# Optimization experiments

Measured on AMD Instinct MI355X. Metric: run time of the kernel, lower is better.

Reference implementation:

```python
import jax, jax.numpy as jnp
import numpy as np

D = 768          # hidden_size
M = 8            # num_patchmerges
B = 16
S = 2048         # non-CLF tokens


def setup_inputs() -> dict:
    key = jax.random.key(0)
    ks = jax.random.split(key, 12)
    std = 0.02
    tokens = jax.random.normal(ks[0], (B, 1 + S, D), dtype=jnp.float32)
    lengths = jnp.maximum(jax.random.randint(ks[1], (B,), 0, S), 1).astype(jnp.int64)
    # PatchMerger: learned queries + layernorm params
    q = jax.random.normal(ks[2], (M, D), dtype=jnp.float32) * std
    ln_scale = jnp.ones((D,), dtype=jnp.float32)
    ln_bias = jnp.zeros((D,), dtype=jnp.float32)
    # mlp1: Linear(3D, D) -> GELU -> Linear(D, D)
    w1a = jax.random.normal(ks[3], (3 * D, D), dtype=jnp.float32) * std
    b1a = jnp.zeros((D,), dtype=jnp.float32)
    w2a = jax.random.normal(ks[4], (D, D), dtype=jnp.float32) * std
    b2a = jnp.zeros((D,), dtype=jnp.float32)
    # mlp2: Linear((1+M)D, D) -> GELU -> Linear(D, D)
    w1b = jax.random.normal(ks[5], ((1 + M) * D, D), dtype=jnp.float32) * std
    b1b = jnp.zeros((D,), dtype=jnp.float32)
    w2b = jax.random.normal(ks[6], (D, D), dtype=jnp.float32) * std
    b2b = jnp.zeros((D,), dtype=jnp.float32)
    return dict(tokens=tokens, lengths=lengths, q=q, ln_scale=ln_scale,
                ln_bias=ln_bias, w1a=w1a, b1a=b1a, w2a=w2a, b2a=b2a,
                w1b=w1b, b1b=b1b, w2b=w2b, b2b=b2b)


def _hpmlp(x, w1, b1, w2, b2):
    h = jax.nn.gelu(x @ w1 + b1, approximate=False)  # dropout=0 -> identity
    return h @ w2 + b2


def _layernorm(x, scale, bias, eps=1e-5):
    mu = jnp.mean(x, axis=-1, keepdims=True)
    var = jnp.var(x, axis=-1, keepdims=True)
    return (x - mu) * jax.lax.rsqrt(var + eps) * scale + bias


def reference(tokens, lengths, q, ln_scale, ln_bias,
              w1a, b1a, w2a, b2a, w1b, b1b, w2b, b2b):
    clf = tokens[:, 0]            # [B, D]
    x = tokens[:, 1:]             # [B, S, D]
    mask = jnp.arange(S)[None, :] < lengths[:, None]   # [B, S]
    mf = mask[..., None].astype(x.dtype)

    # fixed path: masked mean / max / min over valid tokens
    denom = lengths.astype(x.dtype)[:, None]
    mean_p = jnp.sum(x * mf, axis=1) / denom
    max_p = jnp.max(jnp.where(mask[..., None], x, -jnp.inf), axis=1)
    min_p = jnp.min(jnp.where(mask[..., None], x, jnp.inf), axis=1)
    pooled_trad = jnp.concatenate([mean_p, max_p, min_p], axis=-1)  # [B, 3D]
    out_fixed = _hpmlp(pooled_trad, w1a, b1a, w2a, b2a)

    # learned path: PatchMerger (masked attention from M learned queries)
    xn = _layernorm(x, ln_scale, ln_bias)
    scores = jnp.einsum('md,bsd->bms', q, xn) / jnp.sqrt(jnp.asarray(D, x.dtype))
    scores = jnp.where(mask[:, None, :], scores, -jnp.inf)
    attn = jax.nn.softmax(scores, axis=-1)                # [B, M, S]
    merged = jnp.einsum('bms,bsd->bmd', attn, x)          # [B, M, D]
    pooled_learn = jnp.concatenate([merged.reshape(B, M * D), clf], axis=-1)
    out_learn = _hpmlp(pooled_learn, w1b, b1b, w2b, b2b)

    return jnp.concatenate([out_fixed, out_learn], axis=-1)  # [B, 2D]
```

## Files before the change

### kernel.cpp

```cpp
#include <hip/hip_runtime.h>
#include <math.h>

#define SD 768
#define SB 16
#define SM 8
#define SS 2048
#define TOK_ROW 2049
#define NEG_INF (-__builtin_inff())

#define OFF_PPOOL   0
#define OFF_PO      1179648
#define OFF_PML     4325376
#define OFF_PTRAD   4333568
#define OFF_PLEARN  4370432
#define OFF_P1A     4481024
#define OFF_P1B     4702208
#define OFF_HA      5365760
#define OFF_HB      5378048
#define OFF_P2A     5390336
#define OFF_P2B     5464064

__device__ __forceinline__ int clen(int v) { return v < 1 ? 1 : (v > SS ? SS : v); }

__global__ __launch_bounds__(256, 2) void k1_flash(
    const float* __restrict__ tokens, const int* __restrict__ lengths,
    const float* __restrict__ q, const float* __restrict__ lns,
    const float* __restrict__ lnb, float* __restrict__ ppool,
    float* __restrict__ pO, float* __restrict__ pml) {
  int c = blockIdx.x, b = blockIdx.y;
  int len = clen(lengths[b]);
  int c0 = c * 64;
  if (c0 >= len) return;
  int tid = threadIdx.x, w = tid >> 6, lane = tid & 63;
  int mm = lane & 7;

  __shared__ float p_lds[4][16][8];
  __shared__ float pool_lds[4][3][SD];
  __shared__ float O_lds[SM][SD];
  __shared__ float mx_lds[8];

  {
    float* pf = &p_lds[0][0][0];
    for (int i = tid; i < 512; i += 256) pf[i] = NEG_INF;
  }

  float4 qr[8][3];
  float qs1sel, qbsel;
  {
    float4 l4[3], lb4[3];
    #pragma unroll
    for (int g = 0; g < 3; ++g) {
      l4[g] = *(const float4*)(lns + g * 256 + lane * 4);
      lb4[g] = *(const float4*)(lnb + g * 256 + lane * 4);
    }
    float qs1r[8], qbr[8];
    #pragma unroll
    for (int m = 0; m < 8; ++m) {
      float s1 = 0.f, sb = 0.f;
      #pragma unroll
      for (int g = 0; g < 3; ++g) {
        float4 qv = *(const float4*)(q + m * SD + g * 256 + lane * 4);
        float4 qs;
        qs.x = qv.x * l4[g].x; qs.y = qv.y * l4[g].y;
        qs.z = qv.z * l4[g].z; qs.w = qv.w * l4[g].w;
        qr[m][g] = qs;
        s1 += qs.x + qs.y + qs.z + qs.w;
        sb += qv.x * lb4[g].x + qv.y * lb4[g].y + qv.z * lb4[g].z + qv.w * lb4[g].w;
      }
      #pragma unroll
      for (int o = 32; o; o >>= 1) { s1 += __shfl_xor(s1, o, 64); sb += __shfl_xor(sb, o, 64); }
      qs1r[m] = s1; qbr[m] = sb;
    }
    qs1sel = qs1r[0]; qbsel = qbr[0];
    #pragma unroll
    for (int m = 1; m < 8; ++m) {
      qs1sel = (mm == m) ? qs1r[m] : qs1sel;
      qbsel = (mm == m) ? qbr[m] : qbsel;
    }
  }
  __syncthreads();

  float psum[12], pmax[12], pmin[12];
  #pragma unroll
  for (int j = 0; j < 12; ++j) { psum[j] = 0.f; pmax[j] = NEG_INF; pmin[j] = -NEG_INF; }

  int srow = c0 + w * 16;
  int smax = len - srow; if (smax > 16) smax = 16; if (smax < 0) smax = 0;
  const float* xrow = tokens + ((size_t)b * TOK_ROW + 1 + srow) * SD;

  float4 nx0 = {}, nx1 = {}, nx2 = {};
  if (smax > 0) {
    nx0 = *(const float4*)(xrow + lane * 4);
    nx1 = *(const float4*)(xrow + 256 + lane * 4);
    nx2 = *(const float4*)(xrow + 512 + lane * 4);
  }
  for (int i = 0; i < smax; ++i) {
    float4 x0 = nx0, x1 = nx1, x2 = nx2;
    if (i + 1 < smax) {
      const float* xq = xrow + (size_t)(i + 1) * SD;
      nx0 = *(const float4*)(xq + lane * 4);
      nx1 = *(const float4*)(xq + 256 + lane * 4);
      nx2 = *(const float4*)(xq + 512 + lane * 4);
    }
    float xv[12] = {x0.x, x0.y, x0.z, x0.w, x1.x, x1.y, x1.z, x1.w,
                    x2.x, x2.y, x2.z, x2.w};
    float s1 = 0.f, s2 = 0.f;
    #pragma unroll
    for (int j = 0; j < 12; ++j) {
      float v = xv[j];
      psum[j] += v;
      pmax[j] = fmaxf(pmax[j], v);
      pmin[j] = fminf(pmin[j], v);
      s1 += v;
      s2 += v * v;
    }
    float d[8];
    #pragma unroll
    for (int m = 0; m < 8; ++m) {
      float4 a0 = qr[m][0], a1 = qr[m][1], a2 = qr[m][2];
      d[m] = a0.x * xv[0] + a0.y * xv[1] + a0.z * xv[2] + a0.w * xv[3]
           + a1.x * xv[4] + a1.y * xv[5] + a1.z * xv[6] + a1.w * xv[7]
           + a2.x * xv[8] + a2.y * xv[9] + a2.z * xv[10] + a2.w * xv[11];
    }
    #pragma unroll
    for (int o = 1; o <= 4; o <<= 1)
      #pragma unroll
      for (int m = 0; m < 8; ++m) d[m] += __shfl_xor(d[m], o, 64);
    float u = d[0];
    #pragma unroll
    for (int m = 1; m < 8; ++m) u = (mm == m) ? d[m] : u;
    #pragma unroll
    for (int o = 8; o <= 32; o <<= 1) {
      u += __shfl_xor(u, o, 64);
      s1 += __shfl_xor(s1, o, 64);
      s2 += __shfl_xor(s2, o, 64);
    }
    #pragma unroll
    for (int o = 1; o <= 4; o <<= 1) { s1 += __shfl_xor(s1, o, 64); s2 += __shfl_xor(s2, o, 64); }
    float mu = s1 * (1.f / 768.f);
    float var = s2 * (1.f / 768.f) - mu * mu;
    float rstd = rsqrtf(var + 1e-5f);
    float sc = (rstd * u - rstd * mu * qs1sel + qbsel) * 0.03608439182435161f;
    if (lane < 8) p_lds[w][i][lane] = sc;
  }

  #pragma unroll
  for (int g = 0; g < 3; ++g) {
    int dd = g * 256 + lane * 4;
    *(float4*)&pool_lds[w][0][dd] = make_float4(psum[g*4], psum[g*4+1], psum[g*4+2], psum[g*4+3]);
    *(float4*)&pool_lds[w][1][dd] = make_float4(pmax[g*4], pmax[g*4+1], pmax[g*4+2], pmax[g*4+3]);
    *(float4*)&pool_lds[w][2][dd] = make_float4(pmin[g*4], pmin[g*4+1], pmin[g*4+2], pmin[g*4+3]);
  }
  __syncthreads();

  float* pf = &p_lds[0][0][0];
  if (tid < 8) {
    float mxv = NEG_INF;
    for (int r = 0; r < 64; ++r) mxv = fmaxf(mxv, pf[r * 8 + tid]);
    mx_lds[tid] = mxv;
  }
  __syncthreads();
  for (int e = tid; e < 512; e += 256) {
    int m = e & 7;
    pf[e] = __expf(pf[e] - mx_lds[m]);
  }
  __syncthreads();
  if (tid < 8) {
    float lv = 0.f;
    for (int r = 0; r < 64; ++r) lv += pf[r * 8 + tid];
    size_t base = (size_t)(c * SB + b) * 16;
    pml[base + tid] = mx_lds[tid];
    pml[base + 8 + tid] = lv;
  }

  float O[8][12];
  #pragma unroll
  for (int m = 0; m < 8; ++m)
    #pragma unroll
    for (int j = 0; j < 12; ++j) O[m][j] = 0.f;
  float4 a0v = {}, a1v = {}, a2v = {}, b0v = {}, b1v = {}, b2v = {};
  if (smax > 0) {
    a0v = *(const float4*)(xrow + lane * 4);
    a1v = *(const float4*)(xrow + 256 + lane * 4);
    a2v = *(const float4*)(xrow + 512 + lane * 4);
  }
  if (smax > 1) {
    const float* xq = xrow + SD;
    b0v = *(const float4*)(xq + lane * 4);
    b1v = *(const float4*)(xq + 256 + lane * 4);
    b2v = *(const float4*)(xq + 512 + lane * 4);
  }
  for (int i = 0; i < smax; ++i) {
    float4 x0 = a0v, x1 = a1v, x2 = a2v;
    a0v = b0v; a1v = b1v; a2v = b2v;
    if (i + 2 < smax) {
      const float* xq = xrow + (size_t)(i + 2) * SD;
      b0v = *(const float4*)(xq + lane * 4);
      b1v = *(const float4*)(xq + 256 + lane * 4);
      b2v = *(const float4*)(xq + 512 + lane * 4);
    }
    float xv[12] = {x0.x, x0.y, x0.z, x0.w, x1.x, x1.y, x1.z, x1.w,
                    x2.x, x2.y, x2.z, x2.w};
    const float4* pr = (const float4*)&p_lds[w][i][0];
    float4 pa = pr[0], pb = pr[1];
    float pm[8] = {pa.x, pa.y, pa.z, pa.w, pb.x, pb.y, pb.z, pb.w};
    #pragma unroll
    for (int m = 0; m < 8; ++m)
      #pragma unroll
      for (int j = 0; j < 12; ++j) O[m][j] += pm[m] * xv[j];
  }
  #pragma unroll
  for (int r = 0; r < 4; ++r) {
    if (w == r) {
      #pragma unroll
      for (int m = 0; m < 8; ++m)
        #pragma unroll
        for (int g = 0; g < 3; ++g) {
          int dd = g * 256 + lane * 4;
          float4 mine = make_float4(O[m][g*4], O[m][g*4+1], O[m][g*4+2], O[m][g*4+3]);
          if (r == 0) {
            *(float4*)&O_lds[m][dd] = mine;
          } else {
            float4 cur = *(float4*)&O_lds[m][dd];
            cur.x += mine.x; cur.y += mine.y; cur.z += mine.z; cur.w += mine.w;
            *(float4*)&O_lds[m][dd] = cur;
          }
        }
    }
    __syncthreads();
  }

  size_t obase = (size_t)(c * SB + b) * 6144;
  const float* of = &O_lds[0][0];
  for (int j = tid * 4; j < 6144; j += 1024)
    *(float4*)&pO[obase + j] = *(const float4*)&of[j];

  size_t pbase = (size_t)(c * SB + b) * 2304;
  for (int j4 = tid * 4; j4 < 2304; j4 += 1024) {
    int stat = j4 / SD, dd = j4 - stat * SD;
    float4 v0 = *(float4*)&pool_lds[0][stat][dd];
    float4 v1 = *(float4*)&pool_lds[1][stat][dd];
    float4 v2 = *(float4*)&pool_lds[2][stat][dd];
    float4 v3 = *(float4*)&pool_lds[3][stat][dd];
    float4 r;
    if (stat == 0) {
      r.x = v0.x + v1.x + v2.x + v3.x; r.y = v0.y + v1.y + v2.y + v3.y;
      r.z = v0.z + v1.z + v2.z + v3.z; r.w = v0.w + v1.w + v2.w + v3.w;
    } else if (stat == 1) {
      r.x = fmaxf(fmaxf(v0.x, v1.x), fmaxf(v2.x, v3.x));
      r.y = fmaxf(fmaxf(v0.y, v1.y), fmaxf(v2.y, v3.y));
      r.z = fmaxf(fmaxf(v0.z, v1.z), fmaxf(v2.z, v3.z));
      r.w = fmaxf(fmaxf(v0.w, v1.w), fmaxf(v2.w, v3.w));
    } else {
      r.x = fminf(fminf(v0.x, v1.x), fminf(v2.x, v3.x));
      r.y = fminf(fminf(v0.y, v1.y), fminf(v2.y, v3.y));
      r.z = fminf(fminf(v0.z, v1.z), fminf(v2.z, v3.z));
      r.w = fminf(fminf(v0.w, v1.w), fminf(v2.w, v3.w));
    }
    *(float4*)&ppool[pbase + j4] = r;
  }
}

__global__ void k_combine(const float* __restrict__ ppool, const float* __restrict__ pO,
                          const float* __restrict__ pml, const float* __restrict__ tokens,
                          const int* __restrict__ lengths,
                          float* __restrict__ ptrad, float* __restrict__ plearn) {
  int tile = blockIdx.x, b = blockIdx.y;
  int len = clen(lengths[b]);
  int nv = (len + 63) >> 6;
  int tid = threadIdx.x;
  __shared__ float pml_lds[32][16];
  __shared__ float e_lds[32][8];
  __shared__ float Linv_lds[8];
  for (int t = tid; t < nv * 16; t += 256) {
    int cc = t >> 4, j = t & 15;
    pml_lds[cc][j] = pml[(size_t)(cc * SB + b) * 16 + j];
  }
  __syncthreads();
  if (tid < 8) {
    float M = NEG_INF;
    for (int cc = 0; cc < nv; ++cc) M = fmaxf(M, pml_lds[cc][tid]);
    float L = 0.f;
    for (int cc = 0; cc < nv; ++cc) {
      float e = __expf(pml_lds[cc][tid] - M);
      e_lds[cc][tid] = e;
      L += e * pml_lds[cc][8 + tid];
    }
    Linv_lds[tid] = 1.f / L;
  }
  __syncthreads();
  #pragma unroll
  for (int k = 0; k < 4; ++k) {
    int jj = tile * 1024 + k * 256 + tid;
    if (jj < 2304) {
      int stat = jj / SD;
      const float* pp = ppool + jj + (size_t)b * 2304;
      if (stat == 0) {
        float a0 = 0.f, a1 = 0.f, a2 = 0.f, a3 = 0.f;
        int cc = 0;
        for (; cc + 4 <= nv; cc += 4) {
          a0 += pp[(size_t)(cc    ) * SB * 2304];
          a1 += pp[(size_t)(cc + 1) * SB * 2304];
          a2 += pp[(size_t)(cc + 2) * SB * 2304];
          a3 += pp[(size_t)(cc + 3) * SB * 2304];
        }
        for (; cc < nv; ++cc) a0 += pp[(size_t)cc * SB * 2304];
        ptrad[b * 2304 + jj] = ((a0 + a1) + (a2 + a3)) / (float)len;
      } else if (stat == 1) {
        float a0 = NEG_INF, a1 = NEG_INF, a2 = NEG_INF, a3 = NEG_INF;
        int cc = 0;
        for (; cc + 4 <= nv; cc += 4) {
          a0 = fmaxf(a0, pp[(size_t)(cc    ) * SB * 2304]);
          a1 = fmaxf(a1, pp[(size_t)(cc + 1) * SB * 2304]);
          a2 = fmaxf(a2, pp[(size_t)(cc + 2) * SB * 2304]);
          a3 = fmaxf(a3, pp[(size_t)(cc + 3) * SB * 2304]);
        }
        for (; cc < nv; ++cc) a0 = fmaxf(a0, pp[(size_t)cc * SB * 2304]);
        ptrad[b * 2304 + jj] = fmaxf(fmaxf(a0, a1), fmaxf(a2, a3));
      } else {
        float a0 = -NEG_INF, a1 = -NEG_INF, a2 = -NEG_INF, a3 = -NEG_INF;
        int cc = 0;
        for (; cc + 4 <= nv; cc += 4) {
          a0 = fminf(a0, pp[(size_t)(cc    ) * SB * 2304]);
          a1 = fminf(a1, pp[(size_t)(cc + 1) * SB * 2304]);
          a2 = fminf(a2, pp[(size_t)(cc + 2) * SB * 2304]);
          a3 = fminf(a3, pp[(size_t)(cc + 3) * SB * 2304]);
        }
        for (; cc < nv; ++cc) a0 = fminf(a0, pp[(size_t)cc * SB * 2304]);
        ptrad[b * 2304 + jj] = fminf(fminf(a0, a1), fminf(a2, a3));
      }
    } else if (jj < 8448) {
      int t = jj - 2304;
      int m = t / SD;
      const float* po = pO + t + (size_t)b * 6144;
      float a0 = 0.f, a1 = 0.f, a2 = 0.f, a3 = 0.f;
      float a4 = 0.f, a5 = 0.f, a6 = 0.f, a7 = 0.f;
      int cc = 0;
      for (; cc + 8 <= nv; cc += 8) {
        a0 += po[(size_t)(cc    ) * SB * 6144] * e_lds[cc    ][m];
        a1 += po[(size_t)(cc + 1) * SB * 6144] * e_lds[cc + 1][m];
        a2 += po[(size_t)(cc + 2) * SB * 6144] * e_lds[cc + 2][m];
        a3 += po[(size_t)(cc + 3) * SB * 6144] * e_lds[cc + 3][m];
        a4 += po[(size_t)(cc + 4) * SB * 6144] * e_lds[cc + 4][m];
        a5 += po[(size_t)(cc + 5) * SB * 6144] * e_lds[cc + 5][m];
        a6 += po[(size_t)(cc + 6) * SB * 6144] * e_lds[cc + 6][m];
        a7 += po[(size_t)(cc + 7) * SB * 6144] * e_lds[cc + 7][m];
      }
      for (; cc < nv; ++cc) a0 += po[(size_t)cc * SB * 6144] * e_lds[cc][m];
      plearn[b * 6912 + t] = (((a0 + a1) + (a2 + a3)) + ((a4 + a5) + (a6 + a7))) * Linv_lds[m];
    } else {
      int dd = jj - 8448;
      plearn[b * 6912 + 6144 + dd] = tokens[(size_t)b * TOK_ROW * SD + dd];
    }
  }
}

__global__ __launch_bounds__(256) void gemm_partial(
    const float* __restrict__ XA, const float* __restrict__ WA, int ktA, float* __restrict__ PA,
    const float* __restrict__ XB, const float* __restrict__ WB, float* __restrict__ PB) {
  int nt = blockIdx.x, ky = blockIdx.y;
  const float *X, *W; float* P; int kt, ktN;
  if (ky < ktA) { X = XA; W = WA; P = PA; kt = ky; ktN = ktA; }
  else { X = XB; W = WB; P = PB; kt = ky - ktA; ktN = gridDim.y - ktA; }
  int K = ktN * 128;
  int k0 = kt * 128;
  __shared__ __align__(16) float xt[128 * 20];
  __shared__ float red[4][64][17];
  int tid = threadIdx.x;
  int kk = tid & 127, half = tid >> 7;
  #pragma unroll
  for (int u = 0; u < 8; ++u) {
    int b2 = half * 8 + u;
    xt[kk * 20 + b2] = X[b2 * K + k0 + kk];
  }
  __syncthreads();
  int w = tid >> 6, lane = tid & 63;
  int n = nt * 64 + lane;
  float acc[16];
  #pragma unroll
  for (int b2 = 0; b2 < 16; ++b2) acc[b2] = 0.f;
  const float* Wp = W + (size_t)k0 * SD + n;
  #pragma unroll 8
  for (int kj = 0; kj < 32; ++kj) {
    int k = w + kj * 4;
    float wv = Wp[(size_t)k * SD];
    const float4* xr = reinterpret_cast<const float4*>(xt + k * 20);
    float4 a0 = xr[0], a1 = xr[1], a2 = xr[2], a3 = xr[3];
    acc[0] += wv * a0.x; acc[1] += wv * a0.y; acc[2] += wv * a0.z; acc[3] += wv * a0.w;
    acc[4] += wv * a1.x; acc[5] += wv * a1.y; acc[6] += wv * a1.z; acc[7] += wv * a1.w;
    acc[8] += wv * a2.x; acc[9] += wv * a2.y; acc[10] += wv * a2.z; acc[11] += wv * a2.w;
    acc[12] += wv * a3.x; acc[13] += wv * a3.y; acc[14] += wv * a3.z; acc[15] += wv * a3.w;
  }
  #pragma unroll
  for (int b2 = 0; b2 < 16; ++b2) red[w][lane][b2] = acc[b2];
  __syncthreads();
  for (int i = tid; i < 1024; i += 256) {
    int nn = i & 63, b2 = i >> 6;
    float r = red[0][nn][b2] + red[1][nn][b2] + red[2][nn][b2] + red[3][nn][b2];
    P[(size_t)(kt * 16 + b2) * SD + nt * 64 + nn] = r;
  }
}

__global__ void gelu_reduce(const float* __restrict__ PA, const float* __restrict__ b1a,
                            float* __restrict__ HA, const float* __restrict__ PB,
                            const float* __restrict__ b1b, float* __restrict__ HB) {
  int y = blockIdx.y;
  int j = blockIdx.x * 256 + threadIdx.x;
  float r;
  if (y == 0) {
    r = b1a[j % SD];
    #pragma unroll
    for (int kt = 0; kt < 18; ++kt) r += PA[kt * 12288 + j];
    HA[j] = r * 0.5f * (1.f + erff(r * 0.70710678118654752f));
  } else {
    r = b1b[j % SD];
    #pragma unroll
    for (int kt = 0; kt < 54; ++kt) r += PB[kt * 12288 + j];
    HB[j] = r * 0.5f * (1.f + erff(r * 0.70710678118654752f));
  }
}

__global__ void final_reduce(const float* __restrict__ P2A, const float* __restrict__ b2a,
                             const float* __restrict__ P2B, const float* __restrict__ b2b,
                             float* __restrict__ out) {
  int y = blockIdx.y;
  const float* P = y ? P2B : P2A;
  const float* bias = y ? b2b : b2a;
  int j = blockIdx.x * 256 + threadIdx.x;
  float r = bias[j % SD];
  #pragma unroll
  for (int kt = 0; kt < 6; ++kt) r += P[kt * 12288 + j];
  int b = j / SD, nn = j - b * SD;
  out[b * 1536 + y * SD + nn] = r;
}

extern "C" void kernel_launch(void* const* d_in, const int* in_sizes, int n_in,
                              void* d_out, int out_size, void* d_ws, size_t ws_size,
                              hipStream_t stream) {
  const float* tokens = (const float*)d_in[0];
  const int* lengths  = (const int*)d_in[1];
  const float* q      = (const float*)d_in[2];
  const float* lns    = (const float*)d_in[3];
  const float* lnb    = (const float*)d_in[4];
  const float* w1a    = (const float*)d_in[5];
  const float* b1a    = (const float*)d_in[6];
  const float* w2a    = (const float*)d_in[7];
  const float* b2a    = (const float*)d_in[8];
  const float* w1b    = (const float*)d_in[9];
  const float* b1b    = (const float*)d_in[10];
  const float* w2b    = (const float*)d_in[11];
  const float* b2b    = (const float*)d_in[12];
  float* ws  = (float*)d_ws;
  float* out = (float*)d_out;

  float* ppool  = ws + OFF_PPOOL;
  float* pO     = ws + OFF_PO;
  float* pml    = ws + OFF_PML;
  float* ptrad  = ws + OFF_PTRAD;
  float* plearn = ws + OFF_PLEARN;
  float* p1a    = ws + OFF_P1A;
  float* p1b    = ws + OFF_P1B;
  float* ha     = ws + OFF_HA;
  float* hb     = ws + OFF_HB;
  float* p2a    = ws + OFF_P2A;
  float* p2b    = ws + OFF_P2B;

  k1_flash<<<dim3(32, 16), 256, 0, stream>>>(tokens, lengths, q, lns, lnb, ppool, pO, pml);
  k_combine<<<dim3(9, 16), 256, 0, stream>>>(ppool, pO, pml, tokens, lengths, ptrad, plearn);
  gemm_partial<<<dim3(12, 72), 256, 0, stream>>>(ptrad, w1a, 18, p1a, plearn, w1b, p1b);
  gelu_reduce<<<dim3(48, 2), 256, 0, stream>>>(p1a, b1a, ha, p1b, b1b, hb);
  gemm_partial<<<dim3(12, 12), 256, 0, stream>>>(ha, w2a, 6, p2a, hb, w2b, p2b);
  final_reduce<<<dim3(48, 2), 256, 0, stream>>>(p2a, b2a, p2b, b2b, out);
}
```

Before: 232.5 us.

## Fuse combine and MLP stages into one persistent kernel with grid barriers

Merges the combine, first GEMM, GELU reduce, second GEMM and final reduce kernels into a single 864-block kernel. The stages are separated by atomic-counter grid barriers, and the counters are reset by the flash kernel. This removes four kernel launches and their inter-kernel gaps. In exchange it relies on all 864 blocks being co-resident (launch bounds 4 blocks per CU), and most blocks sit idle at the later, smaller stages.

New measurement: 765.7 us. 229% more time.

```diff
diff --git a/kernel.cpp b/kernel.cpp
--- a/kernel.cpp
+++ b/kernel.cpp
@@ -19,15 +19,31 @@
 #define OFF_HB      5378048
 #define OFF_P2A     5390336
 #define OFF_P2B     5464064
+#define OFF_CNT     5537792
+
+#define MEGA_NB 864
 
 __device__ __forceinline__ int clen(int v) { return v < 1 ? 1 : (v > SS ? SS : v); }
+
+__device__ __forceinline__ void gridbar(int* cnt, int target) {
+  __syncthreads();
+  if (threadIdx.x == 0) {
+    __threadfence();
+    __hip_atomic_fetch_add(cnt, 1, __ATOMIC_RELEASE, __HIP_MEMORY_SCOPE_AGENT);
+    while (__hip_atomic_load(cnt, __ATOMIC_ACQUIRE, __HIP_MEMORY_SCOPE_AGENT) < target)
+      __builtin_amdgcn_s_sleep(2);
+    __threadfence();
+  }
+  __syncthreads();
+}
 
 __global__ __launch_bounds__(256, 2) void k1_flash(
     const float* __restrict__ tokens, const int* __restrict__ lengths,
     const float* __restrict__ q, const float* __restrict__ lns,
     const float* __restrict__ lnb, float* __restrict__ ppool,
-    float* __restrict__ pO, float* __restrict__ pml) {
+    float* __restrict__ pO, float* __restrict__ pml, int* __restrict__ cnt) {
   int c = blockIdx.x, b = blockIdx.y;
+  if (c == 0 && b == 0 && threadIdx.x < 4) cnt[threadIdx.x] = 0;
   int len = clen(lengths[b]);
   int c0 = c * 64;
   if (c0 >= len) return;
@@ -261,38 +277,72 @@
   }
 }
 
-__global__ void k_combine(const float* __restrict__ ppool, const float* __restrict__ pO,
-                          const float* __restrict__ pml, const float* __restrict__ tokens,
-                          const int* __restrict__ lengths,
-                          float* __restrict__ ptrad, float* __restrict__ plearn) {
-  int tile = blockIdx.x, b = blockIdx.y;
-  int len = clen(lengths[b]);
-  int nv = (len + 63) >> 6;
-  int tid = threadIdx.x;
-  __shared__ float pml_lds[32][16];
-  __shared__ float e_lds[32][8];
-  __shared__ float Linv_lds[8];
-  for (int t = tid; t < nv * 16; t += 256) {
-    int cc = t >> 4, j = t & 15;
-    pml_lds[cc][j] = pml[(size_t)(cc * SB + b) * 16 + j];
-  }
-  __syncthreads();
-  if (tid < 8) {
-    float M = NEG_INF;
-    for (int cc = 0; cc < nv; ++cc) M = fmaxf(M, pml_lds[cc][tid]);
-    float L = 0.f;
-    for (int cc = 0; cc < nv; ++cc) {
-      float e = __expf(pml_lds[cc][tid] - M);
-      e_lds[cc][tid] = e;
-      L += e * pml_lds[cc][8 + tid];
-    }
-    Linv_lds[tid] = 1.f / L;
-  }
-  __syncthreads();
-  #pragma unroll
-  for (int k = 0; k < 4; ++k) {
-    int jj = tile * 1024 + k * 256 + tid;
-    if (jj < 2304) {
+__device__ __forceinline__ void gemm_tile(const float* __restrict__ X,
+                                          const float* __restrict__ W,
+                                          float* __restrict__ P,
+                                          int kt, int ktN, int nt, int tid,
+                                          float* __restrict__ smem) {
+  float* xt = smem;
+  float* red = smem + 2560;
+  int K = ktN * 128;
+  int k0 = kt * 128;
+  int kk = tid & 127, half = tid >> 7;
+  #pragma unroll
+  for (int u = 0; u < 8; ++u) {
+    int b2 = half * 8 + u;
+    xt[kk * 20 + b2] = X[b2 * K + k0 + kk];
+  }
+  __syncthreads();
+  int w = tid >> 6, lane = tid & 63;
+  int n = nt * 64 + lane;
+  float acc[16];
+  #pragma unroll
+  for (int b2 = 0; b2 < 16; ++b2) acc[b2] = 0.f;
+  const float* Wp = W + (size_t)k0 * SD + n;
+  #pragma unroll 8
+  for (int kj = 0; kj < 32; ++kj) {
+    int k = w + kj * 4;
+    float wv = Wp[(size_t)k * SD];
+    const float4* xr = reinterpret_cast<const float4*>(xt + k * 20);
+    float4 a0 = xr[0], a1 = xr[1], a2 = xr[2], a3 = xr[3];
+    acc[0] += wv * a0.x; acc[1] += wv * a0.y; acc[2] += wv * a0.z; acc[3] += wv * a0.w;
+    acc[4] += wv * a1.x; acc[5] += wv * a1.y; acc[6] += wv * a1.z; acc[7] += wv * a1.w;
+    acc[8] += wv * a2.x; acc[9] += wv * a2.y; acc[10] += wv * a2.z; acc[11] += wv * a2.w;
+    acc[12] += wv * a3.x; acc[13] += wv * a3.y; acc[14] += wv * a3.z; acc[15] += wv * a3.w;
+  }
+  #pragma unroll
+  for (int b2 = 0; b2 < 16; ++b2) red[(w * 64 + lane) * 17 + b2] = acc[b2];
+  __syncthreads();
+  for (int i = tid; i < 1024; i += 256) {
+    int nn = i & 63, b2 = i >> 6;
+    float r = red[nn * 17 + b2] + red[(64 + nn) * 17 + b2]
+            + red[(128 + nn) * 17 + b2] + red[(192 + nn) * 17 + b2];
+    P[(size_t)(kt * 16 + b2) * SD + nt * 64 + nn] = r;
+  }
+}
+
+__global__ __launch_bounds__(256, 4) void k2_mega(
+    const float* __restrict__ ppool, const float* __restrict__ pO,
+    const float* __restrict__ pml, const float* __restrict__ tokens,
+    const int* __restrict__ lengths,
+    const float* __restrict__ w1a, const float* __restrict__ b1a,
+    const float* __restrict__ w2a, const float* __restrict__ b2a,
+    const float* __restrict__ w1b, const float* __restrict__ b1b,
+    const float* __restrict__ w2b, const float* __restrict__ b2b,
+    float* __restrict__ ptrad, float* __restrict__ plearn,
+    float* __restrict__ p1a, float* __restrict__ p1b,
+    float* __restrict__ ha, float* __restrict__ hb,
+    float* __restrict__ p2a, float* __restrict__ p2b,
+    float* __restrict__ out, int* __restrict__ cnt) {
+  __shared__ __align__(16) float smem[6912];
+  int bid = blockIdx.x, tid = threadIdx.x;
+
+  if (bid < 576) {
+    int b = bid / 36, t36 = bid % 36;
+    int len = clen(lengths[b]);
+    int nv = (len + 63) >> 6;
+    int jj = t36 * 256 + tid;
+    if (t36 < 9) {
       int stat = jj / SD;
       const float* pp = ppool + jj + (size_t)b * 2304;
       if (stat == 0) {
@@ -329,109 +379,93 @@
         for (; cc < nv; ++cc) a0 = fminf(a0, pp[(size_t)cc * SB * 2304]);
         ptrad[b * 2304 + jj] = fminf(fminf(a0, a1), fminf(a2, a3));
       }
-    } else if (jj < 8448) {
-      int t = jj - 2304;
-      int m = t / SD;
-      const float* po = pO + t + (size_t)b * 6144;
+    } else if (t36 < 33) {
+      float* pml_l = smem;
+      float* e_l   = smem + 512;
+      float* linv  = smem + 768;
+      for (int t = tid; t < nv * 16; t += 256)
+        pml_l[t] = pml[(size_t)((t >> 4) * SB + b) * 16 + (t & 15)];
+      __syncthreads();
+      if (tid < 8) {
+        float M = NEG_INF;
+        for (int cc = 0; cc < nv; ++cc) M = fmaxf(M, pml_l[cc * 16 + tid]);
+        float L = 0.f;
+        for (int cc = 0; cc < nv; ++cc) {
+          float e = __expf(pml_l[cc * 16 + tid] - M);
+          e_l[cc * 8 + tid] = e;
+          L += e * pml_l[cc * 16 + 8 + tid];
+        }
+        linv[tid] = 1.f / L;
+      }
+      __syncthreads();
+      int t_ = jj - 2304;
+      int m = t_ / SD;
+      const float* po = pO + t_ + (size_t)b * 6144;
       float a0 = 0.f, a1 = 0.f, a2 = 0.f, a3 = 0.f;
       float a4 = 0.f, a5 = 0.f, a6 = 0.f, a7 = 0.f;
       int cc = 0;
       for (; cc + 8 <= nv; cc += 8) {
-        a0 += po[(size_t)(cc    ) * SB * 6144] * e_lds[cc    ][m];
-        a1 += po[(size_t)(cc + 1) * SB * 6144] * e_lds[cc + 1][m];
-        a2 += po[(size_t)(cc + 2) * SB * 6144] * e_lds[cc + 2][m];
-        a3 += po[(size_t)(cc + 3) * SB * 6144] * e_lds[cc + 3][m];
-        a4 += po[(size_t)(cc + 4) * SB * 6144] * e_lds[cc + 4][m];
-        a5 += po[(size_t)(cc + 5) * SB * 6144] * e_lds[cc + 5][m];
-        a6 += po[(size_t)(cc + 6) * SB * 6144] * e_lds[cc + 6][m];
-        a7 += po[(size_t)(cc + 7) * SB * 6144] * e_lds[cc + 7][m];
+        a0 += po[(size_t)(cc    ) * SB * 6144] * e_l[(cc    ) * 8 + m];
+        a1 += po[(size_t)(cc + 1) * SB * 6144] * e_l[(cc + 1) * 8 + m];
+        a2 += po[(size_t)(cc + 2) * SB * 6144] * e_l[(cc + 2) * 8 + m];
+        a3 += po[(size_t)(cc + 3) * SB * 6144] * e_l[(cc + 3) * 8 + m];
+        a4 += po[(size_t)(cc + 4) * SB * 6144] * e_l[(cc + 4) * 8 + m];
+        a5 += po[(size_t)(cc + 5) * SB * 6144] * e_l[(cc + 5) * 8 + m];
+        a6 += po[(size_t)(cc + 6) * SB * 6144] * e_l[(cc + 6) * 8 + m];
+        a7 += po[(size_t)(cc + 7) * SB * 6144] * e_l[(cc + 7) * 8 + m];
       }
-      for (; cc < nv; ++cc) a0 += po[(size_t)cc * SB * 6144] * e_lds[cc][m];
-      plearn[b * 6912 + t] = (((a0 + a1) + (a2 + a3)) + ((a4 + a5) + (a6 + a7))) * Linv_lds[m];
+      for (; cc < nv; ++cc) a0 += po[(size_t)cc * SB * 6144] * e_l[cc * 8 + m];
+      plearn[b * 6912 + t_] = (((a0 + a1) + (a2 + a3)) + ((a4 + a5) + (a6 + a7))) * linv[m];
     } else {
       int dd = jj - 8448;
       plearn[b * 6912 + 6144 + dd] = tokens[(size_t)b * TOK_ROW * SD + dd];
     }
   }
-}
-
-__global__ __launch_bounds__(256) void gemm_partial(
-    const float* __restrict__ XA, const float* __restrict__ WA, int ktA, float* __restrict__ PA,
-    const float* __restrict__ XB, const float* __restrict__ WB, float* __restrict__ PB) {
-  int nt = blockIdx.x, ky = blockIdx.y;
-  const float *X, *W; float* P; int kt, ktN;
-  if (ky < ktA) { X = XA; W = WA; P = PA; kt = ky; ktN = ktA; }
-  else { X = XB; W = WB; P = PB; kt = ky - ktA; ktN = gridDim.y - ktA; }
-  int K = ktN * 128;
-  int k0 = kt * 128;
-  __shared__ __align__(16) float xt[128 * 20];
-  __shared__ float red[4][64][17];
-  int tid = threadIdx.x;
-  int kk = tid & 127, half = tid >> 7;
-  #pragma unroll
-  for (int u = 0; u < 8; ++u) {
-    int b2 = half * 8 + u;
-    xt[kk * 20 + b2] = X[b2 * K + k0 + kk];
-  }
-  __syncthreads();
-  int w = tid >> 6, lane = tid & 63;
-  int n = nt * 64 + lane;
-  float acc[16];
-  #pragma unroll
-  for (int b2 = 0; b2 < 16; ++b2) acc[b2] = 0.f;
-  const float* Wp = W + (size_t)k0 * SD + n;
-  #pragma unroll 8
-  for (int kj = 0; kj < 32; ++kj) {
-    int k = w + kj * 4;
-    float wv = Wp[(size_t)k * SD];
-    const float4* xr = reinterpret_cast<const float4*>(xt + k * 20);
-    float4 a0 = xr[0], a1 = xr[1], a2 = xr[2], a3 = xr[3];
-    acc[0] += wv * a0.x; acc[1] += wv * a0.y; acc[2] += wv * a0.z; acc[3] += wv * a0.w;
-    acc[4] += wv * a1.x; acc[5] += wv * a1.y; acc[6] += wv * a1.z; acc[7] += wv * a1.w;
-    acc[8] += wv * a2.x; acc[9] += wv * a2.y; acc[10] += wv * a2.z; acc[11] += wv * a2.w;
-    acc[12] += wv * a3.x; acc[13] += wv * a3.y; acc[14] += wv * a3.z; acc[15] += wv * a3.w;
-  }
-  #pragma unroll
-  for (int b2 = 0; b2 < 16; ++b2) red[w][lane][b2] = acc[b2];
-  __syncthreads();
-  for (int i = tid; i < 1024; i += 256) {
-    int nn = i & 63, b2 = i >> 6;
-    float r = red[0][nn][b2] + red[1][nn][b2] + red[2][nn][b2] + red[3][nn][b2];
-    P[(size_t)(kt * 16 + b2) * SD + nt * 64 + nn] = r;
-  }
-}
-
-__global__ void gelu_reduce(const float* __restrict__ PA, const float* __restrict__ b1a,
-                            float* __restrict__ HA, const float* __restrict__ PB,
-                            const float* __restrict__ b1b, float* __restrict__ HB) {
-  int y = blockIdx.y;
-  int j = blockIdx.x * 256 + threadIdx.x;
-  float r;
-  if (y == 0) {
-    r = b1a[j % SD];
-    #pragma unroll
-    for (int kt = 0; kt < 18; ++kt) r += PA[kt * 12288 + j];
-    HA[j] = r * 0.5f * (1.f + erff(r * 0.70710678118654752f));
-  } else {
-    r = b1b[j % SD];
-    #pragma unroll
-    for (int kt = 0; kt < 54; ++kt) r += PB[kt * 12288 + j];
-    HB[j] = r * 0.5f * (1.f + erff(r * 0.70710678118654752f));
-  }
-}
-
-__global__ void final_reduce(const float* __restrict__ P2A, const float* __restrict__ b2a,
-                             const float* __restrict__ P2B, const float* __restrict__ b2b,
-                             float* __restrict__ out) {
-  int y = blockIdx.y;
-  const float* P = y ? P2B : P2A;
-  const float* bias = y ? b2b : b2a;
-  int j = blockIdx.x * 256 + threadIdx.x;
-  float r = bias[j % SD];
-  #pragma unroll
-  for (int kt = 0; kt < 6; ++kt) r += P[kt * 12288 + j];
-  int b = j / SD, nn = j - b * SD;
-  out[b * 1536 + y * SD + nn] = r;
+  gridbar(cnt + 0, MEGA_NB);
+
+  {
+    int nt = bid % 12, ky = bid / 12;
+    if (ky < 18) gemm_tile(ptrad, w1a, p1a, ky, 18, nt, tid, smem);
+    else         gemm_tile(plearn, w1b, p1b, ky - 18, 54, nt, tid, smem);
+  }
+  gridbar(cnt + 1, MEGA_NB);
+
+  if (bid < 96) {
+    int y = bid / 48;
+    int j = (bid % 48) * 256 + tid;
+    float r;
+    if (y == 0) {
+      r = b1a[j % SD];
+      #pragma unroll
+      for (int kt = 0; kt < 18; ++kt) r += p1a[kt * 12288 + j];
+      ha[j] = r * 0.5f * (1.f + erff(r * 0.70710678118654752f));
+    } else {
+      r = b1b[j % SD];
+      #pragma unroll
+      for (int kt = 0; kt < 54; ++kt) r += p1b[kt * 12288 + j];
+      hb[j] = r * 0.5f * (1.f + erff(r * 0.70710678118654752f));
+    }
+  }
+  gridbar(cnt + 2, MEGA_NB);
+
+  if (bid < 144) {
+    int nt = bid % 12, ky = bid / 12;
+    if (ky < 6) gemm_tile(ha, w2a, p2a, ky, 6, nt, tid, smem);
+    else        gemm_tile(hb, w2b, p2b, ky - 6, 6, nt, tid, smem);
+  }
+  gridbar(cnt + 3, MEGA_NB);
+
+  if (bid < 96) {
+    int y = bid / 48;
+    const float* P = y ? p2b : p2a;
+    const float* bias = y ? b2b : b2a;
+    int j = (bid % 48) * 256 + tid;
+    float r = bias[j % SD];
+    #pragma unroll
+    for (int kt = 0; kt < 6; ++kt) r += P[kt * 12288 + j];
+    int b = j / SD, nn = j - b * SD;
+    out[b * 1536 + y * SD + nn] = r;
+  }
 }
 
 extern "C" void kernel_launch(void* const* d_in, const int* in_sizes, int n_in,
@@ -464,11 +498,11 @@
   float* hb     = ws + OFF_HB;
   float* p2a    = ws + OFF_P2A;
   float* p2b    = ws + OFF_P2B;
-
-  k1_flash<<<dim3(32, 16), 256, 0, stream>>>(tokens, lengths, q, lns, lnb, ppool, pO, pml);
-  k_combine<<<dim3(9, 16), 256, 0, stream>>>(ppool, pO, pml, tokens, lengths, ptrad, plearn);
-  gemm_partial<<<dim3(12, 72), 256, 0, stream>>>(ptrad, w1a, 18, p1a, plearn, w1b, p1b);
-  gelu_reduce<<<dim3(48, 2), 256, 0, stream>>>(p1a, b1a, ha, p1b, b1b, hb);
-  gemm_partial<<<dim3(12, 12), 256, 0, stream>>>(ha, w2a, 6, p2a, hb, w2b, p2b);
-  final_reduce<<<dim3(48, 2), 256, 0, stream>>>(p2a, b2a, p2b, b2b, out);
+  int*   cnt    = (int*)(ws + OFF_CNT);
+
+  k1_flash<<<dim3(32, 16), 256, 0, stream>>>(tokens, lengths, q, lns, lnb, ppool, pO, pml, cnt);
+  k2_mega<<<dim3(MEGA_NB), 256, 0, stream>>>(ppool, pO, pml, tokens, lengths,
+                                             w1a, b1a, w2a, b2a, w1b, b1b, w2b, b2b,
+                                             ptrad, plearn, p1a, p1b, ha, hb, p2a, p2b,
+                                             out, cnt);
 }
```
